# Kernel tuning notes

Hardware: AMD Instinct MI355X
Metric: run time of the kernel (lower is better)

Reference implementation:

```python
import jax, jax.numpy as jnp
import numpy as np
import math

N, I, C, T, V, M = 256, 2, 6, 300, 25, 2
D = 256
IN_DIM = I * C * T * V * M  # 180000


def _const_mats():
    a = math.radians(30.0)
    ca, sa = math.cos(a), math.sin(a)
    R_x = np.array([[1, 0, 0], [0, ca, sa], [0, -sa, ca]], np.float32).T
    R_y = np.array([[ca, 0, -sa], [0, 1, 0], [sa, 0, ca]], np.float32).T
    R_z = np.array([[ca, sa, 0], [-sa, ca, 0], [0, 0, 1]], np.float32).T
    R_rotate = R_x @ R_y @ R_z
    R_scale = np.diag([2.0, 2.0, 2.0]).astype(np.float32)
    R_shear = np.ones((3, 3), np.float32)  # sh_next=1 -> all ones (transpose is identity op)
    return R_rotate, R_shear, R_scale


def _param_mats():
    rotate_w = np.zeros((3, 3), np.float32)
    rotate_w[0, 0] = 1.0
    rotate_w[1, 1] = rotate_w[1, 2] = rotate_w[2, 1] = rotate_w[2, 2] = 0.7
    shear_w = np.full((3, 3), 0.8, np.float32)
    np.fill_diagonal(shear_w, 1.0)
    scale_w = np.diag([0.6, 0.6, 0.6]).astype(np.float32)
    return rotate_w, shear_w, scale_w


def setup_inputs() -> dict:
    key = jax.random.key(0)
    k1, k2 = jax.random.split(key)
    R_rotate, R_shear, R_scale = _const_mats()
    rotate_w, shear_w, scale_w = _param_mats()
    x = jax.random.normal(k1, (N, I, C, T, V, M), jnp.float32)
    W = jax.random.normal(k2, (IN_DIM, D), jnp.float32) * (1.0 / math.sqrt(IN_DIM))
    b = jnp.zeros((D,), jnp.float32)
    return {
        "x": x,
        "rotate_weight": jnp.asarray(rotate_w),
        "shear_weight": jnp.asarray(shear_w),
        "scale_weight": jnp.asarray(scale_w),
        "W_backbone": W,
        "b_backbone": b,
        "R_rotate": jnp.asarray(R_rotate),
        "R_shear": jnp.asarray(R_shear),
        "R_scale": jnp.asarray(R_scale),
    }


def _loss_fn(q, z, n):
    q = q / jnp.linalg.norm(q, axis=-1, keepdims=True)
    z = z / jnp.linalg.norm(z, axis=-1, keepdims=True)
    sim = q @ z.T                       # [N, N]
    diag = jnp.diagonal(sim)            # (q*z).sum(-1)
    offdiag_sum = sim.sum(axis=-1) - diag
    return diag - offdiag_sum / (n - 1)


def reference(x, rotate_weight, shear_weight, scale_weight, W_backbone, b_backbone,
              R_rotate, R_shear, R_scale):
    n, i, c, t, v, m = x.shape
    # per-pass effective 3x3 matrices (elementwise gated constants)
    Rr = R_rotate * rotate_weight
    Rs = R_shear * shear_weight
    Rc = R_scale * scale_weight
    Rtot = Rr @ Rs @ Rc  # sequential passes compose: y @ Rr @ Rs @ Rc
    # split C=6 into two xyz chunks, rotate coord axis (vectorized over N,I,chunk,T,V,M)
    xr = x.reshape(n, i, 2, 3, t, v, m)
    x_aug = jnp.einsum("nhctvm,cd->nhdtvm", xr.reshape(n * i, 2 * 0 + 2, 3, t, v, m)[0:0] if False else xr.reshape(n, i * 2, 3, t, v, m), Rtot)
    x_aug = x_aug.reshape(n, i, c, t, v, m)
    # torch x1 = x aliases: x2 == x1 == augmented tensor -> both branches identical
    feats = x_aug.reshape(n, -1)
    z = feats @ W_backbone + b_backbone  # backbone; projector(num_layers=0) is identity
    out = z                              # out1 == out2 == z
    q = z                                # predictor is identity
    z_d = jax.lax.stop_gradient(z)
    loss = _loss_fn(q, z_d, n) + _loss_fn(q, z_d, n)
    return (loss.mean(), out, out)
```

## Files before the change

kernel.cpp:

```cpp
#include <hip/hip_runtime.h>

typedef __attribute__((ext_vector_type(4))) short bf16x4;
typedef __attribute__((ext_vector_type(8))) short bf16x8;
typedef __attribute__((ext_vector_type(16))) float f32x16;
typedef __attribute__((ext_vector_type(4))) float f32x4;
typedef __attribute__((ext_vector_type(4))) unsigned int u32x4;

__device__ __forceinline__ unsigned short f2bf(float f) {
    unsigned int u = __builtin_bit_cast(unsigned int, f);
    u += 0x7fffu + ((u >> 16) & 1u);
    return (unsigned short)(u >> 16);
}

#define PA 196

__global__ __launch_bounds__(1024) void gemm_kernel(
    const float* __restrict__ x,
    const float* __restrict__ rw, const float* __restrict__ sw, const float* __restrict__ cw,
    const float* __restrict__ W,
    const float* __restrict__ Rr, const float* __restrict__ Rs, const float* __restrict__ Rc,
    float* __restrict__ P)
{
    __shared__ unsigned short lds_a[256 * PA];
    __shared__ unsigned int   lds_b[2][16 * 256];

    const int tid = threadIdx.x;
    const int blk = blockIdx.x;
    const int p0  = blk * 60;

    float Ar[9], Br[9], Cr[9], T1[9], RT[9];
    #pragma unroll
    for (int e = 0; e < 9; ++e) { Ar[e] = Rr[e]*rw[e]; Br[e] = Rs[e]*sw[e]; Cr[e] = Rc[e]*cw[e]; }
    #pragma unroll
    for (int r = 0; r < 3; ++r)
        #pragma unroll
        for (int c = 0; c < 3; ++c)
            T1[r*3+c] = Ar[r*3+0]*Br[0*3+c] + Ar[r*3+1]*Br[1*3+c] + Ar[r*3+2]*Br[2*3+c];
    #pragma unroll
    for (int r = 0; r < 3; ++r)
        #pragma unroll
        for (int c = 0; c < 3; ++c)
            RT[r*3+c] = T1[r*3+0]*Cr[0*3+c] + T1[r*3+1]*Cr[1*3+c] + T1[r*3+2]*Cr[2*3+c];

    if (tid < 256) {
        bf16x4 zz = (bf16x4)0;
        #pragma unroll
        for (int c3 = 0; c3 < 3; ++c3)
            *((bf16x4*)&lds_a[tid*PA + c3*64 + 60]) = zz;
    }

    const int w  = tid >> 6, l = tid & 63;
    const int lm = l & 31,  lh = l >> 5;
    const int m0 = (w >> 2) * 64;
    const int d0 = (w & 3) * 64;
    const int kp = tid >> 6;
    const int d4 = tid & 63;

    f32x16 acc[2][2];
    #pragma unroll
    for (int fm = 0; fm < 2; ++fm)
        #pragma unroll
        for (int fd = 0; fd < 2; ++fd)
            acc[fm][fd] = (f32x16)0.0f;

    for (int s = 0; s < 4; ++s) {
        const long kbase = (long)(s >> 1) * 90000 + (long)(s & 1) * 45000 + p0;
        const float* xs = x + kbase;

        f32x4 L0 = (f32x4)0.f, L1 = (f32x4)0.f;
        {
            int vk = kp * 2;
            int c3 = vk >> 6, pl = vk & 63;
            if (pl < 60) {
                const float* wr = W + (kbase + (long)c3*15000 + pl)*256 + d4*4;
                L0 = *(const f32x4*)wr;
                L1 = *(const f32x4*)(wr + 256);
            }
        }

        #pragma unroll
        for (int h = 0; h < 2; ++h) {
            f32x4 X[2][3];
            int nn[2], pp[2]; bool act[2];
            #pragma unroll
            for (int u = 0; u < 2; ++u) {
                int idx = (h*2 + u)*1024 + tid;
                act[u] = idx < 3840;
                int n = (int)(((unsigned)idx * 34953u) >> 19);
                int p4 = idx - n*15;
                nn[u] = n; pp[u] = p4;
                if (act[u]) {
                    const float* px = xs + (long)n*180000 + p4*4;
                    X[u][0] = *(const f32x4*)px;
                    X[u][1] = *(const f32x4*)(px + 15000);
                    X[u][2] = *(const f32x4*)(px + 30000);
                }
            }
            #pragma unroll
            for (int u = 0; u < 2; ++u) {
                if (!act[u]) continue;
                bf16x4 o0, o1, o2;
                #pragma unroll
                for (int e = 0; e < 4; ++e) {
                    float x0 = X[u][0][e], x1 = X[u][1][e], x2 = X[u][2][e];
                    o0[e] = (short)f2bf(x0*RT[0] + x1*RT[3] + x2*RT[6]);
                    o1[e] = (short)f2bf(x0*RT[1] + x1*RT[4] + x2*RT[7]);
                    o2[e] = (short)f2bf(x0*RT[2] + x1*RT[5] + x2*RT[8]);
                }
                int a = nn[u]*PA + pp[u]*4;
                *((bf16x4*)&lds_a[a      ]) = o0;
                *((bf16x4*)&lds_a[a +  64]) = o1;
                *((bf16x4*)&lds_a[a + 128]) = o2;
            }
        }

        {
            u32x4 bw;
            #pragma unroll
            for (int e = 0; e < 4; ++e)
                bw[e] = (unsigned int)f2bf(L0[e]) | ((unsigned int)f2bf(L1[e]) << 16);
            *((u32x4*)&lds_b[0][kp*256 + d4*4]) = bw;
        }
        __syncthreads();

        for (int t = 0; t < 6; ++t) {
            f32x4 M0 = (f32x4)0.f, M1 = (f32x4)0.f;
            if (t < 5) {
                int vk = (t+1)*32 + kp*2;
                int c3 = vk >> 6, pl = vk & 63;
                if (pl < 60) {
                    const float* wr = W + (kbase + (long)c3*15000 + pl)*256 + d4*4;
                    M0 = *(const f32x4*)wr;
                    M1 = *(const f32x4*)(wr + 256);
                }
            }

            const unsigned int* bbuf = lds_b[t & 1];
            #pragma unroll
            for (int kk = 0; kk < 2; ++kk) {
                int kb = t*32 + kk*16 + lh*8;
                bf16x8 af[2];
                #pragma unroll
                for (int fm = 0; fm < 2; ++fm) {
                    const unsigned short* pa = &lds_a[(m0 + fm*32 + lm)*PA + kb];
                    bf16x4 alo = *(const bf16x4*)pa;
                    bf16x4 ahi = *(const bf16x4*)(pa + 4);
                    af[fm] = __builtin_shufflevector(alo, ahi, 0,1,2,3,4,5,6,7);
                }
                #pragma unroll
                for (int fd = 0; fd < 2; ++fd) {
                    int db = d0 + fd*32 + lm;
                    int v2 = kk*8 + lh*4;
                    u32x4 bwv = { bbuf[(v2+0)*256 + db], bbuf[(v2+1)*256 + db],
                                  bbuf[(v2+2)*256 + db], bbuf[(v2+3)*256 + db] };
                    bf16x8 bfv = __builtin_bit_cast(bf16x8, bwv);
                    #pragma unroll
                    for (int fm = 0; fm < 2; ++fm)
                        acc[fm][fd] = __builtin_amdgcn_mfma_f32_32x32x16_bf16(af[fm], bfv, acc[fm][fd], 0, 0, 0);
                }
            }

            if (t < 5) {
                u32x4 bw;
                #pragma unroll
                for (int e = 0; e < 4; ++e)
                    bw[e] = (unsigned int)f2bf(M0[e]) | ((unsigned int)f2bf(M1[e]) << 16);
                *((u32x4*)&lds_b[(t+1) & 1][kp*256 + d4*4]) = bw;
            }
            __syncthreads();
        }
    }

    float* Pb = P + (size_t)blk * 65536;
    #pragma unroll
    for (int fm = 0; fm < 2; ++fm)
        #pragma unroll
        for (int fd = 0; fd < 2; ++fd)
            #pragma unroll
            for (int r = 0; r < 16; ++r) {
                int row = m0 + fm*32 + (r & 3) + 8*(r >> 2) + 4*lh;
                int col = d0 + fd*32 + lm;
                Pb[row*256 + col] = acc[fm][fd][r];
            }
}

__global__ __launch_bounds__(512) void reduce_kernel(
    const float* __restrict__ P, const float* __restrict__ bias,
    float* __restrict__ out, float* __restrict__ Z)
{
    __shared__ f32x4 sred[8][64];
    const int n = blockIdx.x;
    const int tid = threadIdx.x;
    const int d4 = tid & 63, sg = tid >> 6;

    const f32x4* p = (const f32x4*)(P + (size_t)n * 256) + d4;
    f32x4 z = (f32x4)0.f;
    #pragma unroll 8
    for (int s = sg; s < 250; s += 8) z += p[(size_t)s * 16384];
    sred[sg][d4] = z;
    __syncthreads();

    if (tid < 64) {
        f32x4 zf = sred[0][tid];
        #pragma unroll
        for (int g = 1; g < 8; ++g) zf += sred[g][tid];
        zf += ((const f32x4*)bias)[tid];
        float* o1 = out + 1 + n*256 + tid*4;
        float* o2 = o1 + 65536;
        #pragma unroll
        for (int e = 0; e < 4; ++e) { o1[e] = zf[e]; o2[e] = zf[e]; }
        float sq = zf[0]*zf[0] + zf[1]*zf[1] + zf[2]*zf[2] + zf[3]*zf[3];
        #pragma unroll
        for (int off = 32; off > 0; off >>= 1) sq += __shfl_xor(sq, off, 64);
        float inv = rsqrtf(sq);
        ((f32x4*)Z)[n*64 + tid] = zf * inv;
    }
}

__global__ __launch_bounds__(1024) void loss_kernel(const float* __restrict__ Z, float* __restrict__ out)
{
    __shared__ f32x4 sp[16][64];
    const int tid = threadIdx.x;
    const int c4 = tid & 63, g = tid >> 6;
    f32x4 S = (f32x4)0.f;
    #pragma unroll 4
    for (int n = g; n < 256; n += 16) S += ((const f32x4*)Z)[n*64 + c4];
    sp[g][c4] = S;
    __syncthreads();
    if (tid < 64) {
        f32x4 T = sp[0][tid];
        #pragma unroll
        for (int gg = 1; gg < 16; ++gg) T += sp[gg][tid];
        float v = T[0]*T[0] + T[1]*T[1] + T[2]*T[2] + T[3]*T[3];
        #pragma unroll
        for (int off = 32; off > 0; off >>= 1) v += __shfl_xor(v, off, 64);
        if (tid == 0)
            out[0] = 2.0f - (2.0f / 255.0f) * (v * (1.0f / 256.0f) - 1.0f);
    }
}

extern "C" void kernel_launch(void* const* d_in, const int* in_sizes, int n_in,
                              void* d_out, int out_size, void* d_ws, size_t ws_size,
                              hipStream_t stream)
{
    (void)in_sizes; (void)n_in; (void)out_size; (void)ws_size;
    const float* x  = (const float*)d_in[0];
    const float* rw = (const float*)d_in[1];
    const float* sw = (const float*)d_in[2];
    const float* cw = (const float*)d_in[3];
    const float* W  = (const float*)d_in[4];
    const float* bb = (const float*)d_in[5];
    const float* Rr = (const float*)d_in[6];
    const float* Rs = (const float*)d_in[7];
    const float* Rc = (const float*)d_in[8];
    float* out = (float*)d_out;
    float* P = (float*)d_ws;
    float* Z = P + (size_t)250 * 65536;

    gemm_kernel<<<250, 1024, 0, stream>>>(x, rw, sw, cw, W, Rr, Rs, Rc, P);
    reduce_kernel<<<256, 512, 0, stream>>>(P, bb, out, Z);
    loss_kernel<<<1, 1024, 0, stream>>>(Z, out);
}
```

Before: 423.3 us.

## Stream W via async global-to-LDS loads with double-buffered 16-wide K strips

The GEMM main loop is restructured into 16 K-strips of 48 (3 coords x 16 positions), each double-buffered for both A and B. W tiles are fetched asynchronously with global_load_lds as fp32 and converted to bf16 at fragment-read time, so the next strip's x and W loads overlap the current strip's MFMAs. The partial-sum layout is changed to [row][block][col] so the reduce kernel reads contiguous memory with fewer threads. In exchange, B now takes fp32 LDS space plus a per-element bf16 conversion inside the inner loop, and there is one barrier per strip.

```diff
diff --git a/kernel.cpp b/kernel.cpp
--- a/kernel.cpp
+++ b/kernel.cpp
@@ -4,7 +4,9 @@
 typedef __attribute__((ext_vector_type(8))) short bf16x8;
 typedef __attribute__((ext_vector_type(16))) float f32x16;
 typedef __attribute__((ext_vector_type(4))) float f32x4;
-typedef __attribute__((ext_vector_type(4))) unsigned int u32x4;
+
+typedef __attribute__((address_space(3))) unsigned int lds_u32_t;
+typedef const __attribute__((address_space(1))) unsigned int glb_u32_t;
 
 __device__ __forceinline__ unsigned short f2bf(float f) {
     unsigned int u = __builtin_bit_cast(unsigned int, f);
@@ -12,7 +14,7 @@
     return (unsigned short)(u >> 16);
 }
 
-#define PA 196
+#define PA2 60
 
 __global__ __launch_bounds__(1024) void gemm_kernel(
     const float* __restrict__ x,
@@ -21,12 +23,18 @@
     const float* __restrict__ Rr, const float* __restrict__ Rs, const float* __restrict__ Rc,
     float* __restrict__ P)
 {
-    __shared__ unsigned short lds_a[256 * PA];
-    __shared__ unsigned int   lds_b[2][16 * 256];
-
-    const int tid = threadIdx.x;
-    const int blk = blockIdx.x;
-    const int p0  = blk * 60;
+    __shared__ unsigned short lds_a[2][256 * PA2];
+    __shared__ float          lds_b[2][48 * 256];
+
+    const int tid  = threadIdx.x;
+    const int blk  = blockIdx.x;
+    const int p0   = blk * 60;
+    const int lane = tid & 63, wv = tid >> 6;
+    const int lm   = lane & 31, lh = lane >> 5;
+    const int m0   = (wv >> 2) * 64;
+    const int d0   = (wv & 3) * 64;
+    const int xn   = tid >> 2;
+    const int xp4  = tid & 3;
 
     float Ar[9], Br[9], Cr[9], T1[9], RT[9];
     #pragma unroll
@@ -42,20 +50,6 @@
         for (int c = 0; c < 3; ++c)
             RT[r*3+c] = T1[r*3+0]*Cr[0*3+c] + T1[r*3+1]*Cr[1*3+c] + T1[r*3+2]*Cr[2*3+c];
 
-    if (tid < 256) {
-        bf16x4 zz = (bf16x4)0;
-        #pragma unroll
-        for (int c3 = 0; c3 < 3; ++c3)
-            *((bf16x4*)&lds_a[tid*PA + c3*64 + 60]) = zz;
-    }
-
-    const int w  = tid >> 6, l = tid & 63;
-    const int lm = l & 31,  lh = l >> 5;
-    const int m0 = (w >> 2) * 64;
-    const int d0 = (w & 3) * 64;
-    const int kp = tid >> 6;
-    const int d4 = tid & 63;
-
     f32x16 acc[2][2];
     #pragma unroll
     for (int fm = 0; fm < 2; ++fm)
@@ -63,149 +57,115 @@
         for (int fd = 0; fd < 2; ++fd)
             acc[fm][fd] = (f32x16)0.0f;
 
-    for (int s = 0; s < 4; ++s) {
-        const long kbase = (long)(s >> 1) * 90000 + (long)(s & 1) * 45000 + p0;
-        const float* xs = x + kbase;
-
-        f32x4 L0 = (f32x4)0.f, L1 = (f32x4)0.f;
-        {
-            int vk = kp * 2;
-            int c3 = vk >> 6, pl = vk & 63;
-            if (pl < 60) {
-                const float* wr = W + (kbase + (long)c3*15000 + pl)*256 + d4*4;
-                L0 = *(const f32x4*)wr;
-                L1 = *(const f32x4*)(wr + 256);
+    f32x4 X0 = (f32x4)0.f, X1 = (f32x4)0.f, X2 = (f32x4)0.f;
+
+    auto issue = [&](int ns) {
+        const int s2 = ns >> 2, j2 = ns & 3;
+        const long kb2 = (long)(s2 >> 1) * 90000 + (long)(s2 & 1) * 45000 + p0;
+        const int pl = j2 * 16 + wv;
+        if (pl < 60) {
+            #pragma unroll
+            for (int q = 0; q < 3; ++q) {
+                glb_u32_t* g = (glb_u32_t*)(W + (kb2 + (long)q * 15000 + pl) * 256 + lane * 4);
+                lds_u32_t* l = (lds_u32_t*)&lds_b[ns & 1][(q * 16 + wv) * 256];
+                __builtin_amdgcn_global_load_lds(g, l, 16, 0, 0);
             }
         }
-
-        #pragma unroll
-        for (int h = 0; h < 2; ++h) {
-            f32x4 X[2][3];
-            int nn[2], pp[2]; bool act[2];
-            #pragma unroll
-            for (int u = 0; u < 2; ++u) {
-                int idx = (h*2 + u)*1024 + tid;
-                act[u] = idx < 3840;
-                int n = (int)(((unsigned)idx * 34953u) >> 19);
-                int p4 = idx - n*15;
-                nn[u] = n; pp[u] = p4;
-                if (act[u]) {
-                    const float* px = xs + (long)n*180000 + p4*4;
-                    X[u][0] = *(const f32x4*)px;
-                    X[u][1] = *(const f32x4*)(px + 15000);
-                    X[u][2] = *(const f32x4*)(px + 30000);
-                }
-            }
-            #pragma unroll
-            for (int u = 0; u < 2; ++u) {
-                if (!act[u]) continue;
-                bf16x4 o0, o1, o2;
+        const bool ok = !(j2 == 3 && xp4 == 3);
+        const float* px = x + kb2 + (long)xn * 180000 + j2 * 16 + xp4 * 4;
+        X0 = ok ? *(const f32x4*)px           : (f32x4)0.f;
+        X1 = ok ? *(const f32x4*)(px + 15000) : (f32x4)0.f;
+        X2 = ok ? *(const f32x4*)(px + 30000) : (f32x4)0.f;
+    };
+
+    auto convertA = [&](int ns) {
+        bf16x4 o0, o1, o2;
+        #pragma unroll
+        for (int e = 0; e < 4; ++e) {
+            float x0 = X0[e], x1 = X1[e], x2 = X2[e];
+            o0[e] = (short)f2bf(x0*RT[0] + x1*RT[3] + x2*RT[6]);
+            o1[e] = (short)f2bf(x0*RT[1] + x1*RT[4] + x2*RT[7]);
+            o2[e] = (short)f2bf(x0*RT[2] + x1*RT[5] + x2*RT[8]);
+        }
+        const int a = xn * PA2 + xp4 * 4;
+        unsigned short* dst = &lds_a[ns & 1][0];
+        *(bf16x4*)&dst[a     ] = o0;
+        *(bf16x4*)&dst[a + 16] = o1;
+        *(bf16x4*)&dst[a + 32] = o2;
+    };
+
+    issue(0);
+    convertA(0);
+    __syncthreads();
+
+    for (int strip = 0; strip < 16; ++strip) {
+        const int cur = strip & 1;
+        const int ns  = strip + 1;
+        if (ns < 16) issue(ns);
+
+        const unsigned short* Ab = &lds_a[cur][0];
+        const float*          Bb = &lds_b[cur][0];
+        #pragma unroll
+        for (int kk = 0; kk < 3; ++kk) {
+            const int kb = kk * 16 + lh * 8;
+            bf16x8 af[2];
+            #pragma unroll
+            for (int fm = 0; fm < 2; ++fm) {
+                const unsigned short* pa = &Ab[(m0 + fm * 32 + lm) * PA2 + kb];
+                bf16x4 alo = *(const bf16x4*)pa;
+                bf16x4 ahi = *(const bf16x4*)(pa + 4);
+                af[fm] = __builtin_shufflevector(alo, ahi, 0,1,2,3,4,5,6,7);
+            }
+            #pragma unroll
+            for (int fd = 0; fd < 2; ++fd) {
+                const int db = d0 + fd * 32 + lm;
+                float bv[8];
                 #pragma unroll
-                for (int e = 0; e < 4; ++e) {
-                    float x0 = X[u][0][e], x1 = X[u][1][e], x2 = X[u][2][e];
-                    o0[e] = (short)f2bf(x0*RT[0] + x1*RT[3] + x2*RT[6]);
-                    o1[e] = (short)f2bf(x0*RT[1] + x1*RT[4] + x2*RT[7]);
-                    o2[e] = (short)f2bf(x0*RT[2] + x1*RT[5] + x2*RT[8]);
-                }
-                int a = nn[u]*PA + pp[u]*4;
-                *((bf16x4*)&lds_a[a      ]) = o0;
-                *((bf16x4*)&lds_a[a +  64]) = o1;
-                *((bf16x4*)&lds_a[a + 128]) = o2;
+                for (int jj = 0; jj < 8; ++jj) bv[jj] = Bb[(kb + jj) * 256 + db];
+                bf16x8 bfv;
+                #pragma unroll
+                for (int jj = 0; jj < 8; ++jj) bfv[jj] = (short)f2bf(bv[jj]);
+                #pragma unroll
+                for (int fm = 0; fm < 2; ++fm)
+                    acc[fm][fd] = __builtin_amdgcn_mfma_f32_32x32x16_bf16(af[fm], bfv, acc[fm][fd], 0, 0, 0);
             }
         }
 
-        {
-            u32x4 bw;
-            #pragma unroll
-            for (int e = 0; e < 4; ++e)
-                bw[e] = (unsigned int)f2bf(L0[e]) | ((unsigned int)f2bf(L1[e]) << 16);
-            *((u32x4*)&lds_b[0][kp*256 + d4*4]) = bw;
-        }
+        if (ns < 16) convertA(ns);
         __syncthreads();
-
-        for (int t = 0; t < 6; ++t) {
-            f32x4 M0 = (f32x4)0.f, M1 = (f32x4)0.f;
-            if (t < 5) {
-                int vk = (t+1)*32 + kp*2;
-                int c3 = vk >> 6, pl = vk & 63;
-                if (pl < 60) {
-                    const float* wr = W + (kbase + (long)c3*15000 + pl)*256 + d4*4;
-                    M0 = *(const f32x4*)wr;
-                    M1 = *(const f32x4*)(wr + 256);
-                }
-            }
-
-            const unsigned int* bbuf = lds_b[t & 1];
-            #pragma unroll
-            for (int kk = 0; kk < 2; ++kk) {
-                int kb = t*32 + kk*16 + lh*8;
-                bf16x8 af[2];
-                #pragma unroll
-                for (int fm = 0; fm < 2; ++fm) {
-                    const unsigned short* pa = &lds_a[(m0 + fm*32 + lm)*PA + kb];
-                    bf16x4 alo = *(const bf16x4*)pa;
-                    bf16x4 ahi = *(const bf16x4*)(pa + 4);
-                    af[fm] = __builtin_shufflevector(alo, ahi, 0,1,2,3,4,5,6,7);
-                }
-                #pragma unroll
-                for (int fd = 0; fd < 2; ++fd) {
-                    int db = d0 + fd*32 + lm;
-                    int v2 = kk*8 + lh*4;
-                    u32x4 bwv = { bbuf[(v2+0)*256 + db], bbuf[(v2+1)*256 + db],
-                                  bbuf[(v2+2)*256 + db], bbuf[(v2+3)*256 + db] };
-                    bf16x8 bfv = __builtin_bit_cast(bf16x8, bwv);
-                    #pragma unroll
-                    for (int fm = 0; fm < 2; ++fm)
-                        acc[fm][fd] = __builtin_amdgcn_mfma_f32_32x32x16_bf16(af[fm], bfv, acc[fm][fd], 0, 0, 0);
-                }
-            }
-
-            if (t < 5) {
-                u32x4 bw;
-                #pragma unroll
-                for (int e = 0; e < 4; ++e)
-                    bw[e] = (unsigned int)f2bf(M0[e]) | ((unsigned int)f2bf(M1[e]) << 16);
-                *((u32x4*)&lds_b[(t+1) & 1][kp*256 + d4*4]) = bw;
-            }
-            __syncthreads();
-        }
     }
 
-    float* Pb = P + (size_t)blk * 65536;
     #pragma unroll
     for (int fm = 0; fm < 2; ++fm)
         #pragma unroll
         for (int fd = 0; fd < 2; ++fd)
             #pragma unroll
             for (int r = 0; r < 16; ++r) {
-                int row = m0 + fm*32 + (r & 3) + 8*(r >> 2) + 4*lh;
-                int col = d0 + fd*32 + lm;
-                Pb[row*256 + col] = acc[fm][fd][r];
-            }
-}
-
-__global__ __launch_bounds__(512) void reduce_kernel(
+                int row = m0 + fm * 32 + (r & 3) + 8 * (r >> 2) + 4 * lh;
+                int col = d0 + fd * 32 + lm;
+                P[((size_t)row * 250 + blk) * 256 + col] = acc[fm][fd][r];
+            }
+}
+
+__global__ __launch_bounds__(256) void reduce_kernel(
     const float* __restrict__ P, const float* __restrict__ bias,
     float* __restrict__ out, float* __restrict__ Z)
 {
-    __shared__ f32x4 sred[8][64];
+    __shared__ f32x4 sred[4][64];
     const int n = blockIdx.x;
     const int tid = threadIdx.x;
     const int d4 = tid & 63, sg = tid >> 6;
 
-    const f32x4* p = (const f32x4*)(P + (size_t)n * 256) + d4;
+    const f32x4* base = (const f32x4*)(P + (size_t)n * 250 * 256);
     f32x4 z = (f32x4)0.f;
-    #pragma unroll 8
-    for (int s = sg; s < 250; s += 8) z += p[(size_t)s * 16384];
+    for (int s = sg; s < 250; s += 4) z += base[s * 64 + d4];
     sred[sg][d4] = z;
     __syncthreads();
 
     if (tid < 64) {
-        f32x4 zf = sred[0][tid];
-        #pragma unroll
-        for (int g = 1; g < 8; ++g) zf += sred[g][tid];
+        f32x4 zf = sred[0][tid] + sred[1][tid] + sred[2][tid] + sred[3][tid];
         zf += ((const f32x4*)bias)[tid];
-        float* o1 = out + 1 + n*256 + tid*4;
+        float* o1 = out + 1 + n * 256 + tid * 4;
         float* o2 = o1 + 65536;
         #pragma unroll
         for (int e = 0; e < 4; ++e) { o1[e] = zf[e]; o2[e] = zf[e]; }
@@ -213,7 +173,7 @@
         #pragma unroll
         for (int off = 32; off > 0; off >>= 1) sq += __shfl_xor(sq, off, 64);
         float inv = rsqrtf(sq);
-        ((f32x4*)Z)[n*64 + tid] = zf * inv;
+        ((f32x4*)Z)[n * 64 + tid] = zf * inv;
     }
 }
 
@@ -224,7 +184,7 @@
     const int c4 = tid & 63, g = tid >> 6;
     f32x4 S = (f32x4)0.f;
     #pragma unroll 4
-    for (int n = g; n < 256; n += 16) S += ((const f32x4*)Z)[n*64 + c4];
+    for (int n = g; n < 256; n += 16) S += ((const f32x4*)Z)[n * 64 + c4];
     sp[g][c4] = S;
     __syncthreads();
     if (tid < 64) {
@@ -255,9 +215,9 @@
     const float* Rc = (const float*)d_in[8];
     float* out = (float*)d_out;
     float* P = (float*)d_ws;
-    float* Z = P + (size_t)250 * 65536;
+    float* Z = P + (size_t)256 * 250 * 256;
 
     gemm_kernel<<<250, 1024, 0, stream>>>(x, rw, sw, cw, W, Rr, Rs, Rc, P);
-    reduce_kernel<<<256, 512, 0, stream>>>(P, bb, out, Z);
+    reduce_kernel<<<256, 256, 0, stream>>>(P, bb, out, Z);
     loss_kernel<<<1, 1024, 0, stream>>>(Z, out);
 }
```

Result: slower. 470.9 us (+11.2%).
